# Kernel tuning notes

Measured on AMD Instinct MI355X. Metric: run time of the kernel, lower is better.

## Reference

```python
import jax, jax.numpy as jnp
import numpy as np

D_MODEL = 1024
NUM_HEADS = 16
HEAD_DIM = D_MODEL // NUM_HEADS


def setup_inputs() -> dict:
    key = jax.random.key(0)
    ks = jax.random.split(key, 10)
    B, SQ, SK = 2, 2048, 2048
    scale = 1.0 / np.sqrt(D_MODEL)
    inp = {
        "x1": jax.random.normal(ks[0], (B, SQ, D_MODEL), jnp.float32),
        "x2": jax.random.normal(ks[1], (B, SK, D_MODEL), jnp.float32),
        "Wq": jax.random.normal(ks[2], (D_MODEL, D_MODEL), jnp.float32) * scale,
        "bq": jnp.zeros((D_MODEL,), jnp.float32),
        "Wk": jax.random.normal(ks[3], (D_MODEL, D_MODEL), jnp.float32) * scale,
        "bk": jnp.zeros((D_MODEL,), jnp.float32),
        "Wv": jax.random.normal(ks[4], (D_MODEL, D_MODEL), jnp.float32) * scale,
        "bv": jnp.zeros((D_MODEL,), jnp.float32),
        "Wo": jax.random.normal(ks[5], (D_MODEL, D_MODEL), jnp.float32) * scale,
        "bo": jnp.zeros((D_MODEL,), jnp.float32),
    }
    return inp


def reference(x1, x2, Wq, bq, Wk, bk, Wv, bv, Wo, bo):
    B, SQ, _ = x1.shape
    SK = x2.shape[1]
    # projections, then split into heads: [B, H, S, Dh]
    def split_heads(t, S):
        return t.reshape(B, S, NUM_HEADS, HEAD_DIM).transpose(0, 2, 1, 3)
    Q = split_heads(x1 @ Wq + bq, SQ)
    K = split_heads(x2 @ Wk + bk, SK)
    V = split_heads(x2 @ Wv + bv, SK)
    # note: original scales by 1/head_dim**0.5
    scores = jnp.einsum("bhqd,bhkd->bhqk", Q, K) / jnp.sqrt(
        jnp.asarray(HEAD_DIM, Q.dtype))
    attn = jax.nn.softmax(scores, axis=-1)
    ctx = jnp.einsum("bhqk,bhkd->bhqd", attn, V)
    ctx = ctx.transpose(0, 2, 1, 3).reshape(B, SQ, D_MODEL)
    return ctx @ Wo + bo
```

## Files before the change

### kernel.cpp

```cpp
#include <hip/hip_runtime.h>
#include <stdint.h>


typedef unsigned short u16b;
typedef __attribute__((ext_vector_type(4))) short short4v;
typedef __attribute__((ext_vector_type(8))) short short8v;
typedef __attribute__((ext_vector_type(4))) float float4v;
typedef __attribute__((ext_vector_type(2))) unsigned int uint2v;

#if __has_builtin(__builtin_amdgcn_exp2f)
__device__ __forceinline__ float exp2_fast(float x){ return __builtin_amdgcn_exp2f(x); }
#else
__device__ __forceinline__ float exp2_fast(float x){ return exp2f(x); }
#endif

__device__ __forceinline__ u16b f2bf(float f) {
  union { float f; unsigned int i; } v; v.f = f;
  return (u16b)((v.i + 0x7fffu + ((v.i >> 16) & 1u)) >> 16);
}
__device__ __forceinline__ void gl_lds16(const u16b* g, u16b* l) {
  __builtin_amdgcn_global_load_lds(
      (const __attribute__((address_space(1))) void*)g,
      (__attribute__((address_space(3))) void*)l, 16, 0, 0);
}

__global__ __launch_bounds__(256) void prep(
    const float* __restrict__ x1, const float* __restrict__ x2,
    const float* __restrict__ W0, const float* __restrict__ W1,
    const float* __restrict__ W2, const float* __restrict__ W3,
    u16b* __restrict__ x1b, u16b* __restrict__ x2b, u16b* __restrict__ WT) {
  const int tid = threadIdx.x;
  const int mode = blockIdx.y;
  if (mode < 2) {
    const float* src = mode ? x2 : x1;
    u16b* dst = mode ? x2b : x1b;
    const int n4 = 1024*1024;
    int i = blockIdx.x * 256 + tid;
    const int stride = gridDim.x * 256;
    for (; i < n4; i += stride) {
      float4v v = ((const float4v*)src)[i];
      short4v o;
      o[0]=(short)f2bf(v[0]); o[1]=(short)f2bf(v[1]);
      o[2]=(short)f2bf(v[2]); o[3]=(short)f2bf(v[3]);
      ((short4v*)dst)[i] = o;
    }
  } else {
    __shared__ u16b tile[32][33];
    const int z = mode - 2;
    const float* src = (z==0) ? W0 : (z==1) ? W1 : (z==2) ? W2 : W3;
    u16b* dst = WT + (size_t)z * (1024*1024);
    const int x = tid & 31, y = tid >> 5;
    const int bx = (blockIdx.x & 31) * 32, by = (blockIdx.x >> 5) * 32;
#pragma unroll
    for (int j=0;j<4;++j)
      tile[y*4+j][x] = f2bf(src[(size_t)(by + y*4+j)*1024 + bx + x]);
    __syncthreads();
#pragma unroll
    for (int j=0;j<4;++j)
      dst[(size_t)(bx + y*4+j)*1024 + by + x] = tile[x][y*4+j];
  }
}

template<int BN, bool OUT_F32, bool BIAS_ROW>
__device__ __forceinline__ void gemm_core(
    u16b* __restrict__ As, u16b* __restrict__ Bs,
    const u16b* __restrict__ A, const u16b* __restrict__ Bt,
    const float* __restrict__ bias, void* __restrict__ Cv,
    int N, int K, int bm, int bn, float oscale) {
  constexpr int NT = BN / 32;
  constexpr int ASTRIDE = 128*64;
  constexpr int BSTRIDE = BN*64;
  const int tid = threadIdx.x;
  const int lane = tid & 63, wave = tid >> 6;
  const int wm = wave >> 1, wn = wave & 1;
  const int l15 = lane & 15, l4 = lane >> 4;
  float4v acc[4][NT];
#pragma unroll
  for (int i=0;i<4;++i)
#pragma unroll
    for (int j=0;j<NT;++j) acc[i][j] = (float4v){0.f,0.f,0.f,0.f};

  auto stage = [&](int buf, int k0) {
#pragma unroll
    for (int j=0;j<4;++j) {
      int idx = j*256 + tid;
      int row = idx >> 3, seg = idx & 7;
      int segg = seg ^ (row & 7);
      gl_lds16(&A[(size_t)(bm+row)*K + k0 + segg*8], &As[buf*ASTRIDE + idx*8]);
    }
#pragma unroll
    for (int j=0;j<BN/32;++j) {
      int idx = j*256 + tid;
      int row = idx >> 3, seg = idx & 7;
      int segg = seg ^ (row & 7);
      gl_lds16(&Bt[(size_t)(bn+row)*K + k0 + segg*8], &Bs[buf*BSTRIDE + idx*8]);
    }
  };

  const int NK = K >> 6;
  stage(0, 0);
  __syncthreads();
  for (int kt = 0; kt < NK; ++kt) {
    const int cur = kt & 1;
    if (kt + 1 < NK) stage(cur ^ 1, (kt + 1) << 6);
    const u16b* Asb = As + cur*ASTRIDE;
    const u16b* Bsb = Bs + cur*BSTRIDE;
#pragma unroll
    for (int ks=0; ks<2; ++ks) {
      short8v af[4], bf[NT];
      const int cs = ((ks*4 + l4) ^ (l15 & 7)) * 8;
#pragma unroll
      for (int mt=0;mt<4;++mt)
        af[mt] = *(const short8v*)&Asb[(wm*64+mt*16+l15)*64 + cs];
#pragma unroll
      for (int nt=0;nt<NT;++nt)
        bf[nt] = *(const short8v*)&Bsb[(wn*(BN/2)+nt*16+l15)*64 + cs];
#pragma unroll
      for (int mt=0;mt<4;++mt)
#pragma unroll
        for (int nt=0;nt<NT;++nt)
          acc[mt][nt] = __builtin_amdgcn_mfma_f32_16x16x32_bf16(af[mt], bf[nt], acc[mt][nt], 0, 0, 0);
    }
    __syncthreads();
  }

#pragma unroll
  for (int nt=0;nt<NT;++nt) {
    int col = bn + wn*(BN/2) + nt*16 + l15;
    float bbc = BIAS_ROW ? 0.f : bias[col];
#pragma unroll
    for (int mt=0;mt<4;++mt) {
      int row0 = bm + wm*64 + mt*16 + l4*4;
#pragma unroll
      for (int r=0;r<4;++r) {
        float bb = BIAS_ROW ? bias[row0+r] : bbc;
        float v = (acc[mt][nt][r] + bb) * oscale;
        if (OUT_F32) ((float*)Cv)[(size_t)(row0+r)*N + col] = v;
        else         ((u16b*)Cv)[(size_t)(row0+r)*N + col] = f2bf(v);
      }
    }
  }
}

__global__ __launch_bounds__(256) void gemm_qkv(
    const u16b* __restrict__ x1b, const u16b* __restrict__ x2b,
    const u16b* __restrict__ WT, const float* __restrict__ bq,
    const float* __restrict__ bk, const float* __restrict__ bv,
    u16b* __restrict__ QKV) {
  __shared__ __align__(16) u16b As[2*128*64];
  __shared__ __align__(16) u16b Bs[2*128*64];
  const int f = blockIdx.x;
  const int xcd = f & 7, s = f >> 3;
  const int z = s >> 5, t = s & 31;
  const size_t Mi = 1024*1024;
  const float QSCALE = 0.125f * 1.4426950408889634f;
  if (z == 2) {
    int bm = (t & 7) * 128;
    int bn = (xcd*4 + (t >> 3)) * 128;
    gemm_core<128,false,true>(As, Bs, WT + 2*Mi, x2b, bv, QKV + 8*Mi,
                              4096, 1024, bm, bn, 1.0f);
  } else {
    int bm = (xcd*4 + (t >> 3)) * 128;
    int bn = (t & 7) * 128;
    gemm_core<128,false,false>(As, Bs, z ? x2b : x1b, WT + (size_t)z*Mi,
                               z ? bk : bq, QKV + (size_t)z*4*Mi,
                               1024, 1024, bm, bn, z ? 1.0f : QSCALE);
  }
}

__global__ __launch_bounds__(256) void gemm_out(
    const u16b* __restrict__ A, const u16b* __restrict__ Bt,
    const float* __restrict__ bias, float* __restrict__ C) {
  __shared__ __align__(16) u16b As[2*128*64];
  __shared__ __align__(16) u16b Bs[2*64*64];
  const int f = blockIdx.x;
  const int xcd = f & 7, s = f >> 3;
  const int bm = (xcd*4 + (s >> 4)) * 128;
  const int bn = (s & 15) * 64;
  gemm_core<64,true,false>(As, Bs, A, Bt, bias, C, 1024, 1024, bm, bn, 1.0f);
}

__device__ __forceinline__ void attn_load(
    const u16b* __restrict__ Kgb, const u16b* __restrict__ Vtb,
    int kvoff, int tid, short8v kreg[4], short8v vreg[4]) {
#pragma unroll
  for (int j=0; j<4; ++j) {
    int idx = j*256 + tid;
    int rowk = idx >> 3, segk = idx & 7;
    kreg[j] = *(const short8v*)&Kgb[(size_t)(kvoff+rowk)*1024 + ((segk ^ (rowk & 7))*8)];
    int rowv = idx >> 4, segv = idx & 15;
    vreg[j] = *(const short8v*)&Vtb[(size_t)rowv*4096 + kvoff + ((segv ^ (rowv & 15))*8)];
  }
}

__global__ __launch_bounds__(256, 2) void attn_q128(
    const u16b* __restrict__ Q, const u16b* __restrict__ Kg,
    const u16b* __restrict__ Vt, u16b* __restrict__ O) {
  __shared__ __align__(16) u16b Ks[128*64];
  __shared__ __align__(16) u16b Vs[64*128];
  __shared__ __align__(16) u16b Ps[4*2*1024];
  const int tid = threadIdx.x;
  const int lane = tid & 63, wave = tid >> 6;
  const int l15 = lane & 15, l4 = lane >> 4;
  const int bh = blockIdx.x;
  const int b = bh >> 4, h = bh & 15;
  const int q0 = blockIdx.y * 128;
  const size_t seqbase = (size_t)b * 2048;
  const int colh = h * 64;
  const u16b* Kgb = Kg + seqbase*1024 + colh;
  const u16b* Vtb = Vt + (size_t)(h*64)*4096 + (size_t)b*2048;
  u16b* Pw = Ps + wave * 2048;

  short8v kreg[4], vreg[4];
  attn_load(Kgb, Vtb, 0, tid, kreg, vreg);

  short8v qf[2][2];
#pragma unroll
  for (int g=0; g<2; ++g) {
    size_t qrow = seqbase + q0 + wave*32 + g*16 + l15;
#pragma unroll
    for (int ks=0; ks<2; ++ks)
      qf[g][ks] = *(const short8v*)&Q[qrow*1024 + colh + ks*32 + l4*8];
  }

  short8v ones;
#pragma unroll
  for (int i=0;i<8;++i) ones[i] = (short)0x3F80;

  float4v lacc[2] = {(float4v){0.f,0.f,0.f,0.f}, (float4v){0.f,0.f,0.f,0.f}};
  float4v oacc[2][4];
#pragma unroll
  for (int g=0; g<2; ++g)
#pragma unroll
    for (int nb=0; nb<4; ++nb) oacc[g][nb] = (float4v){0.f,0.f,0.f,0.f};

  for (int kt = 0; kt < 16; ++kt) {
    __syncthreads();
#pragma unroll
    for (int j=0; j<4; ++j) {
      int idx = j*256 + tid;
      *(short8v*)&Ks[idx*8] = kreg[j];
      *(short8v*)&Vs[idx*8] = vreg[j];
    }
    __syncthreads();
    if (kt < 15)
      attn_load(Kgb, Vtb, (kt+1)*128, tid, kreg, vreg);

    float4v sacc[2][8];
#pragma unroll
    for (int g=0; g<2; ++g)
#pragma unroll
      for (int nb=0; nb<8; ++nb) sacc[g][nb] = (float4v){0.f,0.f,0.f,0.f};
#pragma unroll
    for (int nb=0; nb<8; ++nb)
#pragma unroll
      for (int ks=0; ks<2; ++ks) {
        short8v kf = *(const short8v*)&Ks[(nb*16+l15)*64 + (((ks*4+l4) ^ (l15 & 7))*8)];
        sacc[0][nb] = __builtin_amdgcn_mfma_f32_16x16x32_bf16(kf, qf[0][ks], sacc[0][nb], 0, 0, 0);
        sacc[1][nb] = __builtin_amdgcn_mfma_f32_16x16x32_bf16(kf, qf[1][ks], sacc[1][nb], 0, 0, 0);
      }

#pragma unroll
    for (int h2=0; h2<2; ++h2) {
#pragma unroll
      for (int g=0; g<2; ++g)
#pragma unroll
        for (int nbl=0; nbl<4; ++nbl) {
          const float4v s4 = sacc[g][h2*4 + nbl];
          unsigned int u0 = __float_as_uint(exp2_fast(s4[0]));
          unsigned int u1 = __float_as_uint(exp2_fast(s4[1]));
          unsigned int u2 = __float_as_uint(exp2_fast(s4[2]));
          unsigned int u3 = __float_as_uint(exp2_fast(s4[3]));
          uint2v dw;
          dw[0] = (u0 >> 16) | (u1 & 0xFFFF0000u);
          dw[1] = (u2 >> 16) | (u3 & 0xFFFF0000u);
          *(uint2v*)&Pw[g*1024 + l15*64 + (((nbl*4 + l4) ^ l15)*4)] = dw;
        }
      asm volatile("s_waitcnt lgkmcnt(0)" ::: "memory");

#pragma unroll
      for (int ks2=0; ks2<2; ++ks2) {
        short8v pf[2];
#pragma unroll
        for (int g=0; g<2; ++g) {
          int c0 = (ks2*8 + l4*2) ^ l15;
          int c1 = (ks2*8 + l4*2 + 1) ^ l15;
          short4v pa = *(const short4v*)&Pw[g*1024 + l15*64 + c0*4];
          short4v pb = *(const short4v*)&Pw[g*1024 + l15*64 + c1*4];
          short8v p;
          p[0]=pa[0]; p[1]=pa[1]; p[2]=pa[2]; p[3]=pa[3];
          p[4]=pb[0]; p[5]=pb[1]; p[6]=pb[2]; p[7]=pb[3];
          pf[g] = p;
          lacc[g] = __builtin_amdgcn_mfma_f32_16x16x32_bf16(p, ones, lacc[g], 0, 0, 0);
        }
#pragma unroll
        for (int nb=0; nb<4; ++nb) {
          int cc = (h2*8 + ks2*4 + l4) ^ l15;
          short8v vf = *(const short8v*)&Vs[(nb*16+l15)*128 + cc*8];
          oacc[0][nb] = __builtin_amdgcn_mfma_f32_16x16x32_bf16(pf[0], vf, oacc[0][nb], 0, 0, 0);
          oacc[1][nb] = __builtin_amdgcn_mfma_f32_16x16x32_bf16(pf[1], vf, oacc[1][nb], 0, 0, 0);
        }
      }
    }
  }

#pragma unroll
  for (int g=0; g<2; ++g)
#pragma unroll
    for (int r=0; r<4; ++r) {
      float inv = 1.0f / lacc[g][r];
      size_t row = seqbase + q0 + wave*32 + g*16 + l4*4 + r;
#pragma unroll
      for (int nb=0; nb<4; ++nb)
        O[row*1024 + colh + nb*16 + l15] = f2bf(oacc[g][nb][r] * inv);
    }
}

extern "C" void kernel_launch(void* const* d_in, const int* in_sizes, int n_in,
                              void* d_out, int out_size, void* d_ws, size_t ws_size,
                              hipStream_t stream) {
  const float* x1 = (const float*)d_in[0];
  const float* x2 = (const float*)d_in[1];
  const float* Wq = (const float*)d_in[2];
  const float* bq = (const float*)d_in[3];
  const float* Wk = (const float*)d_in[4];
  const float* bk = (const float*)d_in[5];
  const float* Wv = (const float*)d_in[6];
  const float* bv = (const float*)d_in[7];
  const float* Wo = (const float*)d_in[8];
  const float* bo = (const float*)d_in[9];
  (void)in_sizes; (void)n_in; (void)out_size; (void)ws_size;

  u16b* ws = (u16b*)d_ws;
  const size_t Mi = 1024*1024;
  u16b* WT  = ws;
  u16b* WoT = ws + 3*Mi;
  u16b* x1b = ws + 4*Mi;
  u16b* x2b = ws + 8*Mi;
  u16b* QKV = ws + 12*Mi;
  u16b* Qb  = QKV;
  u16b* Kb  = QKV + 4*Mi;
  u16b* Vtb = QKV + 8*Mi;
  u16b* Cx  = x1b;

  prep<<<dim3(1024,6), 256, 0, stream>>>(x1, x2, Wq, Wk, Wv, Wo, x1b, x2b, WT);

  gemm_qkv<<<dim3(768), 256, 0, stream>>>(x1b, x2b, WT, bq, bk, bv, QKV);

  attn_q128<<<dim3(32,16), 256, 0, stream>>>(Qb, Kb, Vtb, Cx);

  gemm_out<<<dim3(512), 256, 0, stream>>>(Cx, WoT, bo, (float*)d_out);
}
```

Baseline: 219.0 us.

## Replace QKV GEMM with 256x256-tile 8-wave kernel and split-phase pipelining

Replaces the 128x128 QKV projection GEMM with a 256x256-tile kernel using 512 threads. Each K step is split into four quadrant phases, and global-to-LDS staging of the next tile halves is interleaved with MFMA work using explicit waitcnt, barriers and setprio. Larger tiles raise data reuse per LDS load and cut global traffic. The cost is only 192 blocks (fewer than the CU count), higher register and LDS pressure, and more complex synchronisation.

```diff
diff --git a/kernel.cpp b/kernel.cpp
--- a/kernel.cpp
+++ b/kernel.cpp
@@ -23,6 +23,13 @@
       (const __attribute__((address_space(1))) void*)g,
       (__attribute__((address_space(3))) void*)l, 16, 0, 0);
 }
+
+#define FENCE_BARRIER() do { asm volatile("" ::: "memory"); \
+  __builtin_amdgcn_s_barrier(); asm volatile("" ::: "memory"); } while(0)
+#define LGKM0() do { asm volatile("s_waitcnt lgkmcnt(0)" ::: "memory"); \
+  __builtin_amdgcn_sched_barrier(0); } while(0)
+#define VMCNT(n) do { asm volatile("s_waitcnt vmcnt(" #n ")" ::: "memory"); \
+  __builtin_amdgcn_sched_barrier(0); } while(0)
 
 __global__ __launch_bounds__(256) void prep(
     const float* __restrict__ x1, const float* __restrict__ x2,
@@ -61,6 +68,192 @@
   }
 }
 
+template<bool BIAS_ROW>
+__device__ __forceinline__ void gemm256_core(
+    u16b* __restrict__ As, u16b* __restrict__ Bs,
+    const u16b* __restrict__ A, const u16b* __restrict__ Bt,
+    const float* __restrict__ bias, u16b* __restrict__ C,
+    int N, int K, int bm, int bn, float oscale) {
+  constexpr int ASTR = 256*64, BSTR = 256*64;
+  const int tid = threadIdx.x;
+  const int lane = tid & 63, wave = tid >> 6;
+  const int wr = wave >> 2, wc = wave & 3;
+  const int l15 = lane & 15, l4 = lane >> 4;
+
+  auto stage_half = [&](const u16b* __restrict__ G, int row0, int k0,
+                        u16b* __restrict__ Lbase) {
+#pragma unroll
+    for (int j=0;j<2;++j) {
+      int idx = j*512 + tid;
+      int row = idx >> 3, seg = idx & 7;
+      int segg = seg ^ (row & 7);
+      gl_lds16(&G[(size_t)(row0+row)*K + k0 + segg*8], &Lbase[idx*8]);
+    }
+  };
+
+  float4v acc[2][2][4][2];
+#pragma unroll
+  for (int qm=0;qm<2;++qm)
+#pragma unroll
+  for (int qn=0;qn<2;++qn)
+#pragma unroll
+  for (int m=0;m<4;++m)
+#pragma unroll
+  for (int n=0;n<2;++n) acc[qm][qn][m][n] = (float4v){0.f,0.f,0.f,0.f};
+
+  const int NK = K >> 6;
+  stage_half(A,  bm+0,   0,  As + 0);
+  stage_half(Bt, bn+0,   0,  Bs + 0);
+  stage_half(A,  bm+128, 0,  As + 128*64);
+  stage_half(Bt, bn+128, 0,  Bs + 128*64);
+  stage_half(A,  bm+0,   64, As + ASTR);
+  stage_half(Bt, bn+0,   64, Bs + BSTR);
+  VMCNT(4);
+  FENCE_BARRIER();
+
+  int cur = 0;
+  for (int t = 0; t < NK; ++t) {
+    u16b* Ac = As + cur*ASTR;  u16b* Bc = Bs + cur*BSTR;
+    u16b* An = As + (cur^1)*ASTR;  u16b* Bn = Bs + (cur^1)*BSTR;
+    const int k1 = (t+1) << 6, k2 = (t+2) << 6;
+    short8v af[4][2], bf0[2][2], bf1[2][2];
+
+#pragma unroll
+    for (int m=0;m<4;++m)
+#pragma unroll
+      for (int ks=0;ks<2;++ks)
+        af[m][ks] = *(const short8v*)&Ac[(0*128 + wr*64 + m*16 + l15)*64
+                                         + (((ks*4+l4) ^ (l15&7))*8)];
+#pragma unroll
+    for (int n=0;n<2;++n)
+#pragma unroll
+      for (int ks=0;ks<2;++ks)
+        bf0[n][ks] = *(const short8v*)&Bc[(0*128 + wc*32 + n*16 + l15)*64
+                                          + (((ks*4+l4) ^ (l15&7))*8)];
+    if (t+1 < NK) stage_half(A, bm+128, k1, An + 128*64);
+    FENCE_BARRIER();
+    LGKM0();
+    __builtin_amdgcn_s_setprio(1);
+#pragma unroll
+    for (int m=0;m<4;++m)
+#pragma unroll
+      for (int n=0;n<2;++n)
+#pragma unroll
+        for (int ks=0;ks<2;++ks)
+          acc[0][0][m][n] = __builtin_amdgcn_mfma_f32_16x16x32_bf16(
+              af[m][ks], bf0[n][ks], acc[0][0][m][n], 0, 0, 0);
+    __builtin_amdgcn_s_setprio(0);
+    FENCE_BARRIER();
+
+#pragma unroll
+    for (int n=0;n<2;++n)
+#pragma unroll
+      for (int ks=0;ks<2;++ks)
+        bf1[n][ks] = *(const short8v*)&Bc[(1*128 + wc*32 + n*16 + l15)*64
+                                          + (((ks*4+l4) ^ (l15&7))*8)];
+    if (t+1 < NK) stage_half(Bt, bn+128, k1, Bn + 128*64);
+    FENCE_BARRIER();
+    LGKM0();
+    __builtin_amdgcn_s_setprio(1);
+#pragma unroll
+    for (int m=0;m<4;++m)
+#pragma unroll
+      for (int n=0;n<2;++n)
+#pragma unroll
+        for (int ks=0;ks<2;++ks)
+          acc[0][1][m][n] = __builtin_amdgcn_mfma_f32_16x16x32_bf16(
+              af[m][ks], bf1[n][ks], acc[0][1][m][n], 0, 0, 0);
+    __builtin_amdgcn_s_setprio(0);
+    FENCE_BARRIER();
+
+#pragma unroll
+    for (int m=0;m<4;++m)
+#pragma unroll
+      for (int ks=0;ks<2;++ks)
+        af[m][ks] = *(const short8v*)&Ac[(1*128 + wr*64 + m*16 + l15)*64
+                                         + (((ks*4+l4) ^ (l15&7))*8)];
+    if (t+2 < NK) stage_half(A, bm+0, k2, Ac + 0);
+    FENCE_BARRIER();
+    LGKM0();
+    __builtin_amdgcn_s_setprio(1);
+#pragma unroll
+    for (int m=0;m<4;++m)
+#pragma unroll
+      for (int n=0;n<2;++n)
+#pragma unroll
+        for (int ks=0;ks<2;++ks)
+          acc[1][0][m][n] = __builtin_amdgcn_mfma_f32_16x16x32_bf16(
+              af[m][ks], bf0[n][ks], acc[1][0][m][n], 0, 0, 0);
+    __builtin_amdgcn_s_setprio(0);
+    FENCE_BARRIER();
+
+    if (t+2 < NK) stage_half(Bt, bn+0, k2, Bc + 0);
+    FENCE_BARRIER();
+    LGKM0();
+    __builtin_amdgcn_s_setprio(1);
+#pragma unroll
+    for (int m=0;m<4;++m)
+#pragma unroll
+      for (int n=0;n<2;++n)
+#pragma unroll
+        for (int ks=0;ks<2;++ks)
+          acc[1][1][m][n] = __builtin_amdgcn_mfma_f32_16x16x32_bf16(
+              af[m][ks], bf1[n][ks], acc[1][1][m][n], 0, 0, 0);
+    __builtin_amdgcn_s_setprio(0);
+    if (t == NK-2) { VMCNT(0); }
+    else          { VMCNT(4); }
+    FENCE_BARRIER();
+    cur ^= 1;
+  }
+
+#pragma unroll
+  for (int qm=0;qm<2;++qm)
+#pragma unroll
+  for (int qn=0;qn<2;++qn)
+#pragma unroll
+  for (int n=0;n<2;++n) {
+    int col = bn + qn*128 + wc*32 + n*16 + l15;
+    float bbc = BIAS_ROW ? 0.f : bias[col];
+#pragma unroll
+    for (int m=0;m<4;++m) {
+      int row0 = bm + qm*128 + wr*64 + m*16 + l4*4;
+#pragma unroll
+      for (int r=0;r<4;++r) {
+        float bb = BIAS_ROW ? bias[row0+r] : bbc;
+        float v = (acc[qm][qn][m][n][r] + bb) * oscale;
+        C[(size_t)(row0+r)*N + col] = f2bf(v);
+      }
+    }
+  }
+}
+
+__global__ __launch_bounds__(512, 2) void gemm_qkv256(
+    const u16b* __restrict__ x1b, const u16b* __restrict__ x2b,
+    const u16b* __restrict__ WT, const float* __restrict__ bq,
+    const float* __restrict__ bk, const float* __restrict__ bv,
+    u16b* __restrict__ QKV) {
+  __shared__ __align__(16) u16b As[2*256*64];
+  __shared__ __align__(16) u16b Bs[2*256*64];
+  const int f = blockIdx.x;
+  const int z = f >> 6;
+  const int u = f & 63;
+  const int w = ((u & 7) << 3) | (u >> 3);
+  const size_t Mi = 1024*1024;
+  const float QSCALE = 0.125f * 1.4426950408889634f;
+  if (z == 2) {
+    int bm = (w >> 4) * 256;
+    int bn = (w & 15) * 256;
+    gemm256_core<true>(As, Bs, WT + 2*Mi, x2b, bv, QKV + 8*Mi,
+                       4096, 1024, bm, bn, 1.0f);
+  } else {
+    int bm = (w >> 2) * 256;
+    int bn = (w & 3) * 256;
+    gemm256_core<false>(As, Bs, z ? x2b : x1b, WT + (size_t)z*Mi,
+                        z ? bk : bq, QKV + (size_t)z*4*Mi,
+                        1024, 1024, bm, bn, z ? 1.0f : QSCALE);
+  }
+}
+
 template<int BN, bool OUT_F32, bool BIAS_ROW>
 __device__ __forceinline__ void gemm_core(
     u16b* __restrict__ As, u16b* __restrict__ Bs,
@@ -139,32 +332,6 @@
         else         ((u16b*)Cv)[(size_t)(row0+r)*N + col] = f2bf(v);
       }
     }
-  }
-}
-
-__global__ __launch_bounds__(256) void gemm_qkv(
-    const u16b* __restrict__ x1b, const u16b* __restrict__ x2b,
-    const u16b* __restrict__ WT, const float* __restrict__ bq,
-    const float* __restrict__ bk, const float* __restrict__ bv,
-    u16b* __restrict__ QKV) {
-  __shared__ __align__(16) u16b As[2*128*64];
-  __shared__ __align__(16) u16b Bs[2*128*64];
-  const int f = blockIdx.x;
-  const int xcd = f & 7, s = f >> 3;
-  const int z = s >> 5, t = s & 31;
-  const size_t Mi = 1024*1024;
-  const float QSCALE = 0.125f * 1.4426950408889634f;
-  if (z == 2) {
-    int bm = (t & 7) * 128;
-    int bn = (xcd*4 + (t >> 3)) * 128;
-    gemm_core<128,false,true>(As, Bs, WT + 2*Mi, x2b, bv, QKV + 8*Mi,
-                              4096, 1024, bm, bn, 1.0f);
-  } else {
-    int bm = (xcd*4 + (t >> 3)) * 128;
-    int bn = (t & 7) * 128;
-    gemm_core<128,false,false>(As, Bs, z ? x2b : x1b, WT + (size_t)z*Mi,
-                               z ? bk : bq, QKV + (size_t)z*4*Mi,
-                               1024, 1024, bm, bn, z ? 1.0f : QSCALE);
   }
 }
 
@@ -345,7 +512,7 @@
 
   prep<<<dim3(1024,6), 256, 0, stream>>>(x1, x2, Wq, Wk, Wv, Wo, x1b, x2b, WT);
 
-  gemm_qkv<<<dim3(768), 256, 0, stream>>>(x1b, x2b, WT, bq, bk, bv, QKV);
+  gemm_qkv256<<<dim3(192), 512, 0, stream>>>(x1b, x2b, WT, bq, bk, bv, QKV);
 
   attn_q128<<<dim3(32,16), 256, 0, stream>>>(Qb, Kb, Vtb, Cx);
 
```

After: 200.6 us. 1.09x faster.
